# Performance work log

Measured on AMD Instinct MI355X. Metric: run time of the kernel, lower is better.

Reference implementation:

```python
import jax, jax.numpy as jnp
import numpy as np

N_NODES = 50000
N_EDGES = 65536
D_NODE = 1024
D_HID = 1024


def setup_inputs() -> dict:
    key = jax.random.key(0)
    k1, k2, k3, k4, k5 = jax.random.split(key, 5)
    node_feats = jax.random.normal(k1, (N_NODES, D_NODE), dtype=jnp.float32)
    src = jax.random.randint(k2, (N_EDGES,), 0, N_NODES, dtype=jnp.int64)
    dst = jax.random.randint(k3, (N_EDGES,), 0, N_NODES, dtype=jnp.int64)
    # MLP([2048, 1024, 1024]) with ReLU between layers, bias, no BN, no dropout
    W1 = jax.random.normal(k4, (2 * D_NODE, D_HID), dtype=jnp.float32) * (1.0 / np.sqrt(2 * D_NODE))
    b1 = jnp.zeros((D_HID,), dtype=jnp.float32)
    W2 = jax.random.normal(k5, (D_HID, D_HID), dtype=jnp.float32) * (1.0 / np.sqrt(D_HID))
    b2 = jnp.zeros((D_HID,), dtype=jnp.float32)
    return {"node_feats": node_feats, "src": src, "dst": dst,
            "W1": W1, "b1": b1, "W2": W2, "b2": b2}


def reference(node_feats, src, dst, W1, b1, W2, b2):
    # gather per-edge src/dst node features and concat: [E, 2d]
    feat = jnp.concatenate([node_feats[src], node_feats[dst]], axis=1)
    # edge MLP: Linear -> ReLU -> Linear
    h = jax.nn.relu(feat @ W1 + b1)
    e_f = h @ W2 + b2  # [E, D_HID]
    return e_f
```

## Files before the change

kernel.cpp:

```cpp
#include <hip/hip_runtime.h>
#include <stdint.h>
#include <stddef.h>

typedef unsigned short u16;
typedef __bf16 bf16_t;
typedef bf16_t bf16x8 __attribute__((ext_vector_type(8)));
typedef float f32x4 __attribute__((ext_vector_type(4)));
typedef u16 u16x4 __attribute__((ext_vector_type(4)));

#define N_NODES 50000
#define N_EDGES 65536
#define D_NODE 1024
#define D_HID 1024

#define BM 256
#define BK 64
#define BUFE (BM * BK)
#define LDS_BYTES (4 * BUFE * 2)


__device__ __forceinline__ u16 f2bf(float f) {
  union { float f; uint32_t u; } v; v.f = f;
  uint32_t u = v.u;
  u += 0x7FFF + ((u >> 16) & 1);
  return (u16)(u >> 16);
}

typedef __attribute__((address_space(1))) const void GV;
typedef __attribute__((address_space(3))) void LV;

__device__ __forceinline__ void gll16(const void* g, void* lds_wave_base) {
  __builtin_amdgcn_global_load_lds((GV*)g, (LV*)lds_wave_base, 16, 0, 0);
}


__global__ void detect_i64_kernel(const int* __restrict__ src, int* __restrict__ flag) {
  if (threadIdx.x == 0 && blockIdx.x == 0) {
    int o = 0;
    for (int i = 1; i < 32; i += 2) o |= src[i];
    *flag = (o == 0) ? 1 : 0;
  }
}

__global__ void cvt_bf16_kernel(const float* __restrict__ in, u16* __restrict__ out, size_t n4) {
  size_t i = (size_t)blockIdx.x * blockDim.x + threadIdx.x;
  if (i >= n4) return;
  float4 v = reinterpret_cast<const float4*>(in)[i];
  u16x4 o;
  o.x = f2bf(v.x); o.y = f2bf(v.y); o.z = f2bf(v.z); o.w = f2bf(v.w);
  reinterpret_cast<u16x4*>(out)[i] = o;
}

__global__ void transpose_cvt_kernel(const float* __restrict__ in, u16* __restrict__ out,
                                     int K, int N) {
  __shared__ float tile[32][33];
  int n0 = blockIdx.x * 32, k0 = blockIdx.y * 32;
  int tx = threadIdx.x, ty = threadIdx.y;
  #pragma unroll
  for (int i = ty; i < 32; i += 8)
    tile[i][tx] = in[(size_t)(k0 + i) * N + (n0 + tx)];
  __syncthreads();
  #pragma unroll
  for (int i = ty; i < 32; i += 8)
    out[(size_t)(n0 + i) * K + (k0 + tx)] = f2bf(tile[tx][i]);
}


#define PHASE_MFMA(i0, i1)                                                              \
  do {                                                                                  \
    _Pragma("unroll")                                                                   \
    for (int j = 0; j < 4; ++j) {                                                       \
      acc[i0][j] = __builtin_amdgcn_mfma_f32_16x16x32_bf16(afA[0], bfr[j][0], acc[i0][j], 0, 0, 0); \
      acc[i0][j] = __builtin_amdgcn_mfma_f32_16x16x32_bf16(afA[1], bfr[j][1], acc[i0][j], 0, 0, 0); \
    }                                                                                   \
    _Pragma("unroll")                                                                   \
    for (int j = 0; j < 4; ++j) {                                                       \
      acc[i1][j] = __builtin_amdgcn_mfma_f32_16x16x32_bf16(afB[0], bfr[j][0], acc[i1][j], 0, 0, 0); \
      acc[i1][j] = __builtin_amdgcn_mfma_f32_16x16x32_bf16(afB[1], bfr[j][1], acc[i1][j], 0, 0, 0); \
    }                                                                                   \
  } while (0)

#define LDA(dst, i, ks) \
  dst = *reinterpret_cast<const bf16x8*>(As_c + arow + (i) * 16 * BK + ((ks) ? kb1 : kb0))
#define LDB(j, ks) \
  bfr[j][ks] = *reinterpret_cast<const bf16x8*>(Bs_c + brow + (j) * 16 * BK + ((ks) ? kb1 : kb0))

template <bool FIRST>
__launch_bounds__(512, 2)
__global__ void gemm_kernel(const u16* __restrict__ Abf,
                            const int* __restrict__ src,
                            const int* __restrict__ dst,
                            const int* __restrict__ is64p,
                            const u16* __restrict__ Bt,
                            const float* __restrict__ bias,
                            u16* __restrict__ hout,
                            float* __restrict__ fout,
                            const int K) {
  extern __shared__ __align__(16) u16 lds[];
  u16* const ldsA = lds;
  u16* const ldsB = lds + 2 * BUFE;

  const int t = threadIdx.x;
  const int lane = t & 63;
  const int wave = t >> 6;

  const int b = blockIdx.x;
  const int wgid = (b & 7) * 128 + (b >> 3);
  const int bm = (wgid >> 2) * BM;
  const int bn = (wgid & 3) * BM;

  const int wm = (wave >> 2) * 128;
  const int wn = (wave & 3) * 64;

  const int srow = t >> 3;
  const int kswz = (((t & 7) ^ (srow & 7)) << 3);
  const int stoff = wave * 512;

  const u16* ap[4];
  const u16* ad[4];
  const u16* bp[4];
  if constexpr (FIRST) {
    const int is64 = *is64p;
    #pragma unroll
    for (int q = 0; q < 4; ++q) {
      const int e = bm + q * 64 + srow;
      const int s = is64 ? src[2 * e] : src[e];
      const int d = is64 ? dst[2 * e] : dst[e];
      ap[q] = Abf + (size_t)s * D_NODE + kswz;
      ad[q] = Abf + (size_t)d * D_NODE + kswz;
    }
  } else {
    #pragma unroll
    for (int q = 0; q < 4; ++q) {
      ap[q] = Abf + (size_t)(bm + q * 64 + srow) * K + kswz;
      ad[q] = nullptr;
    }
  }
  #pragma unroll
  for (int q = 0; q < 4; ++q)
    bp[q] = Bt + (size_t)(bn + q * 64 + srow) * K + kswz;

  auto stageA = [&](int buf, int q, int u) {
    const u16* g;
    if constexpr (FIRST) {
      g = (u < (D_NODE / BK)) ? (ap[q] + u * BK) : (ad[q] + (u - D_NODE / BK) * BK);
    } else {
      g = ap[q] + u * BK;
    }
    gll16(g, ldsA + buf * BUFE + q * 4096 + stoff);
  };
  auto stageB = [&](int buf, int q, int u) {
    gll16(bp[q] + u * BK, ldsB + buf * BUFE + q * 4096 + stoff);
  };

  const int lm = lane & 15;
  const int kq8 = ((lane >> 4) & 3) << 3;
  const int swzr = (lm & 7) << 3;
  const int kb0 = kq8 ^ swzr;
  const int kb1 = (32 + kq8) ^ swzr;
  const int arow = (wm + lm) * BK;
  const int brow = (wn + lm) * BK;

  f32x4 acc[8][4] = {};

  const int NT = K / BK;

  #pragma unroll
  for (int q = 0; q < 4; ++q) stageB(0, q, 0);
  #pragma unroll
  for (int q = 0; q < 4; ++q) stageA(0, q, 0);
  #pragma unroll
  for (int q = 0; q < 4; ++q) stageB(1, q, 1);
  stageA(1, 0, 1);
  stageA(1, 2, 1);
  asm volatile("s_waitcnt vmcnt(6)" ::: "memory");
  __builtin_amdgcn_s_barrier();

  for (int u = 0; u < NT; ++u) {
    const int cb = u & 1;
    const u16* As_c = ldsA + cb * BUFE;
    const u16* Bs_c = ldsB + cb * BUFE;

    bf16x8 bfr[4][2];
    bf16x8 afA[2], afB[2];

    #pragma unroll
    for (int j = 0; j < 4; ++j) { LDB(j, 0); LDB(j, 1); }
    LDA(afA[0], 0, 0); LDA(afA[1], 0, 1);
    LDA(afB[0], 1, 0); LDA(afB[1], 1, 1);
    if (u + 1 < NT) { stageA(cb ^ 1, 1, u + 1); stageA(cb ^ 1, 3, u + 1); }
    __builtin_amdgcn_s_barrier();
    asm volatile("s_waitcnt lgkmcnt(0)");
    __builtin_amdgcn_s_setprio(1);
    PHASE_MFMA(0, 1);
    __builtin_amdgcn_s_setprio(0);
    __builtin_amdgcn_s_barrier();

    LDA(afA[0], 2, 0); LDA(afA[1], 2, 1);
    LDA(afB[0], 3, 0); LDA(afB[1], 3, 1);
    if (u + 2 < NT) { stageB(cb, 0, u + 2); stageB(cb, 1, u + 2); }
    __builtin_amdgcn_s_barrier();
    asm volatile("s_waitcnt lgkmcnt(0)");
    __builtin_amdgcn_s_setprio(1);
    PHASE_MFMA(2, 3);
    __builtin_amdgcn_s_setprio(0);
    __builtin_amdgcn_s_barrier();

    LDA(afA[0], 4, 0); LDA(afA[1], 4, 1);
    LDA(afB[0], 5, 0); LDA(afB[1], 5, 1);
    if (u + 2 < NT) { stageB(cb, 2, u + 2); stageB(cb, 3, u + 2); }
    __builtin_amdgcn_s_barrier();
    asm volatile("s_waitcnt lgkmcnt(0)");
    __builtin_amdgcn_s_setprio(1);
    PHASE_MFMA(4, 5);
    __builtin_amdgcn_s_setprio(0);
    __builtin_amdgcn_s_barrier();

    LDA(afA[0], 6, 0); LDA(afA[1], 6, 1);
    LDA(afB[0], 7, 0); LDA(afB[1], 7, 1);
    if (u + 2 < NT) { stageA(cb, 0, u + 2); stageA(cb, 2, u + 2); }
    __builtin_amdgcn_s_barrier();
    asm volatile("s_waitcnt lgkmcnt(0)");
    __builtin_amdgcn_s_setprio(1);
    PHASE_MFMA(6, 7);
    __builtin_amdgcn_s_setprio(0);
    if (u + 2 < NT)      asm volatile("s_waitcnt vmcnt(6)" ::: "memory");
    else if (u + 1 < NT) asm volatile("s_waitcnt vmcnt(0)" ::: "memory");
    __builtin_amdgcn_s_barrier();
  }

  const int rq = ((lane >> 4) & 3) * 4;
  #pragma unroll
  for (int j = 0; j < 4; ++j) {
    const int n = bn + wn + 16 * j + lm;
    const float bj = bias[n];
    #pragma unroll
    for (int i = 0; i < 8; ++i) {
      const int m0 = bm + wm + 16 * i + rq;
      f32x4 c = acc[i][j];
      #pragma unroll
      for (int rr = 0; rr < 4; ++rr) {
        float v = c[rr] + bj;
        if (FIRST) {
          v = fmaxf(v, 0.0f);
          hout[(size_t)(m0 + rr) * D_HID + n] = f2bf(v);
        } else {
          fout[(size_t)(m0 + rr) * D_HID + n] = v;
        }
      }
    }
  }
}


extern "C" void kernel_launch(void* const* d_in, const int* in_sizes, int n_in,
                              void* d_out, int out_size, void* d_ws, size_t ws_size,
                              hipStream_t stream) {
  const float* node_feats = (const float*)d_in[0];
  const int*   src        = (const int*)d_in[1];
  const int*   dst        = (const int*)d_in[2];
  const float* W1         = (const float*)d_in[3];
  const float* b1         = (const float*)d_in[4];
  const float* W2         = (const float*)d_in[5];
  const float* b2         = (const float*)d_in[6];
  float* out = (float*)d_out;

  u16* ws = (u16*)d_ws;
  const size_t NODE_E = (size_t)N_NODES * D_NODE;
  u16* node_bf = ws;
  u16* W1T = node_bf + NODE_E;
  u16* W2T = W1T + (size_t)2048 * 1024;
  u16* h   = W2T + (size_t)1024 * 1024;
  int* flag = (int*)(h + (size_t)N_EDGES * D_HID);

  static bool attr_set = false;
  if (!attr_set) {
    hipFuncSetAttribute(reinterpret_cast<const void*>(&gemm_kernel<true>),
                        hipFuncAttributeMaxDynamicSharedMemorySize, LDS_BYTES);
    hipFuncSetAttribute(reinterpret_cast<const void*>(&gemm_kernel<false>),
                        hipFuncAttributeMaxDynamicSharedMemorySize, LDS_BYTES);
    attr_set = true;
  }

  detect_i64_kernel<<<1, 64, 0, stream>>>(src, flag);

  cvt_bf16_kernel<<<(unsigned)(NODE_E / 4 / 256), 256, 0, stream>>>(node_feats, node_bf, NODE_E / 4);

  transpose_cvt_kernel<<<dim3(1024 / 32, 2048 / 32), dim3(32, 8), 0, stream>>>(W1, W1T, 2048, 1024);
  transpose_cvt_kernel<<<dim3(1024 / 32, 1024 / 32), dim3(32, 8), 0, stream>>>(W2, W2T, 1024, 1024);

  gemm_kernel<true><<<1024, 512, LDS_BYTES, stream>>>(
      node_bf, src, dst, flag, W1T, b1, h, nullptr, 2 * D_NODE);

  gemm_kernel<false><<<1024, 512, LDS_BYTES, stream>>>(
      h, nullptr, nullptr, nullptr, W2T, b2, nullptr, out, D_HID);
}
```

Baseline: 822.0 us.

## Simplify GEMM main loop to single-barrier double buffering with one-tile prefetch

Replaces the four-phase interleaved schedule with a simpler loop. The old loop had several barriers per K-tile and a two-tile-ahead prefetch. The new loop issues all A and B global-to-LDS loads for the next tile at the top of the iteration, then runs the MFMAs in three groups split by K-half, and ends with a full vmcnt(0) wait and one barrier. The goal is to cut barrier and synchronisation overhead. The cost is shallower prefetch depth, and global loads are no longer interleaved with compute phases, so gather latency may be exposed. The templated kernel is also wrapped into two non-template entry kernels.

```diff
diff --git a/kernel.cpp b/kernel.cpp
--- a/kernel.cpp
+++ b/kernel.cpp
@@ -66,36 +66,16 @@
 }
 
 
-#define PHASE_MFMA(i0, i1)                                                              \
-  do {                                                                                  \
-    _Pragma("unroll")                                                                   \
-    for (int j = 0; j < 4; ++j) {                                                       \
-      acc[i0][j] = __builtin_amdgcn_mfma_f32_16x16x32_bf16(afA[0], bfr[j][0], acc[i0][j], 0, 0, 0); \
-      acc[i0][j] = __builtin_amdgcn_mfma_f32_16x16x32_bf16(afA[1], bfr[j][1], acc[i0][j], 0, 0, 0); \
-    }                                                                                   \
-    _Pragma("unroll")                                                                   \
-    for (int j = 0; j < 4; ++j) {                                                       \
-      acc[i1][j] = __builtin_amdgcn_mfma_f32_16x16x32_bf16(afB[0], bfr[j][0], acc[i1][j], 0, 0, 0); \
-      acc[i1][j] = __builtin_amdgcn_mfma_f32_16x16x32_bf16(afB[1], bfr[j][1], acc[i1][j], 0, 0, 0); \
-    }                                                                                   \
-  } while (0)
-
-#define LDA(dst, i, ks) \
-  dst = *reinterpret_cast<const bf16x8*>(As_c + arow + (i) * 16 * BK + ((ks) ? kb1 : kb0))
-#define LDB(j, ks) \
-  bfr[j][ks] = *reinterpret_cast<const bf16x8*>(Bs_c + brow + (j) * 16 * BK + ((ks) ? kb1 : kb0))
-
 template <bool FIRST>
-__launch_bounds__(512, 2)
-__global__ void gemm_kernel(const u16* __restrict__ Abf,
-                            const int* __restrict__ src,
-                            const int* __restrict__ dst,
-                            const int* __restrict__ is64p,
-                            const u16* __restrict__ Bt,
-                            const float* __restrict__ bias,
-                            u16* __restrict__ hout,
-                            float* __restrict__ fout,
-                            const int K) {
+__device__ __forceinline__ void gemm_body(const u16* __restrict__ Abf,
+                                          const int* __restrict__ src,
+                                          const int* __restrict__ dst,
+                                          const int* __restrict__ is64p,
+                                          const u16* __restrict__ Bt,
+                                          const float* __restrict__ bias,
+                                          u16* __restrict__ hout,
+                                          float* __restrict__ fout,
+                                          const int K) {
   extern __shared__ __align__(16) u16 lds[];
   u16* const ldsA = lds;
   u16* const ldsB = lds + 2 * BUFE;
@@ -166,14 +146,10 @@
   const int NT = K / BK;
 
   #pragma unroll
+  for (int q = 0; q < 4; ++q) stageA(0, q, 0);
+  #pragma unroll
   for (int q = 0; q < 4; ++q) stageB(0, q, 0);
-  #pragma unroll
-  for (int q = 0; q < 4; ++q) stageA(0, q, 0);
-  #pragma unroll
-  for (int q = 0; q < 4; ++q) stageB(1, q, 1);
-  stageA(1, 0, 1);
-  stageA(1, 2, 1);
-  asm volatile("s_waitcnt vmcnt(6)" ::: "memory");
+  asm volatile("s_waitcnt vmcnt(0)" ::: "memory");
   __builtin_amdgcn_s_barrier();
 
   for (int u = 0; u < NT; ++u) {
@@ -181,51 +157,67 @@
     const u16* As_c = ldsA + cb * BUFE;
     const u16* Bs_c = ldsB + cb * BUFE;
 
-    bf16x8 bfr[4][2];
-    bf16x8 afA[2], afB[2];
-
-    #pragma unroll
-    for (int j = 0; j < 4; ++j) { LDB(j, 0); LDB(j, 1); }
-    LDA(afA[0], 0, 0); LDA(afA[1], 0, 1);
-    LDA(afB[0], 1, 0); LDA(afB[1], 1, 1);
-    if (u + 1 < NT) { stageA(cb ^ 1, 1, u + 1); stageA(cb ^ 1, 3, u + 1); }
-    __builtin_amdgcn_s_barrier();
-    asm volatile("s_waitcnt lgkmcnt(0)");
+    if (u + 1 < NT) {
+      const int nb = cb ^ 1;
+      stageA(nb, 0, u + 1); stageA(nb, 1, u + 1);
+      stageA(nb, 2, u + 1); stageA(nb, 3, u + 1);
+      stageB(nb, 0, u + 1); stageB(nb, 1, u + 1);
+      stageB(nb, 2, u + 1); stageB(nb, 3, u + 1);
+    }
+
+    bf16x8 aq[4], ar[4], bq[4], br[4];
+
+    #pragma unroll
+    for (int j = 0; j < 4; ++j)
+      bq[j] = *reinterpret_cast<const bf16x8*>(Bs_c + brow + j * 1024 + kb0);
+    #pragma unroll
+    for (int i = 0; i < 4; ++i)
+      aq[i] = *reinterpret_cast<const bf16x8*>(As_c + arow + i * 1024 + kb0);
+    #pragma unroll
+    for (int i = 0; i < 4; ++i)
+      ar[i] = *reinterpret_cast<const bf16x8*>(As_c + arow + (i + 4) * 1024 + kb0);
+
     __builtin_amdgcn_s_setprio(1);
-    PHASE_MFMA(0, 1);
+    #pragma unroll
+    for (int i = 0; i < 4; ++i)
+      #pragma unroll
+      for (int j = 0; j < 4; ++j)
+        acc[i][j] = __builtin_amdgcn_mfma_f32_16x16x32_bf16(aq[i], bq[j], acc[i][j], 0, 0, 0);
     __builtin_amdgcn_s_setprio(0);
-    __builtin_amdgcn_s_barrier();
-
-    LDA(afA[0], 2, 0); LDA(afA[1], 2, 1);
-    LDA(afB[0], 3, 0); LDA(afB[1], 3, 1);
-    if (u + 2 < NT) { stageB(cb, 0, u + 2); stageB(cb, 1, u + 2); }
-    __builtin_amdgcn_s_barrier();
-    asm volatile("s_waitcnt lgkmcnt(0)");
+
+    #pragma unroll
+    for (int j = 0; j < 4; ++j)
+      br[j] = *reinterpret_cast<const bf16x8*>(Bs_c + brow + j * 1024 + kb1);
+    #pragma unroll
+    for (int i = 0; i < 4; ++i)
+      aq[i] = *reinterpret_cast<const bf16x8*>(As_c + arow + i * 1024 + kb1);
+
     __builtin_amdgcn_s_setprio(1);
-    PHASE_MFMA(2, 3);
+    #pragma unroll
+    for (int i = 0; i < 4; ++i)
+      #pragma unroll
+      for (int j = 0; j < 4; ++j)
+        acc[i + 4][j] = __builtin_amdgcn_mfma_f32_16x16x32_bf16(ar[i], bq[j], acc[i + 4][j], 0, 0, 0);
     __builtin_amdgcn_s_setprio(0);
-    __builtin_amdgcn_s_barrier();
-
-    LDA(afA[0], 4, 0); LDA(afA[1], 4, 1);
-    LDA(afB[0], 5, 0); LDA(afB[1], 5, 1);
-    if (u + 2 < NT) { stageB(cb, 2, u + 2); stageB(cb, 3, u + 2); }
-    __builtin_amdgcn_s_barrier();
-    asm volatile("s_waitcnt lgkmcnt(0)");
+
+    #pragma unroll
+    for (int i = 0; i < 4; ++i)
+      ar[i] = *reinterpret_cast<const bf16x8*>(As_c + arow + (i + 4) * 1024 + kb1);
+
     __builtin_amdgcn_s_setprio(1);
-    PHASE_MFMA(4, 5);
+    #pragma unroll
+    for (int i = 0; i < 4; ++i)
+      #pragma unroll
+      for (int j = 0; j < 4; ++j)
+        acc[i][j] = __builtin_amdgcn_mfma_f32_16x16x32_bf16(aq[i], br[j], acc[i][j], 0, 0, 0);
+    #pragma unroll
+    for (int i = 0; i < 4; ++i)
+      #pragma unroll
+      for (int j = 0; j < 4; ++j)
+        acc[i + 4][j] = __builtin_amdgcn_mfma_f32_16x16x32_bf16(ar[i], br[j], acc[i + 4][j], 0, 0, 0);
     __builtin_amdgcn_s_setprio(0);
-    __builtin_amdgcn_s_barrier();
-
-    LDA(afA[0], 6, 0); LDA(afA[1], 6, 1);
-    LDA(afB[0], 7, 0); LDA(afB[1], 7, 1);
-    if (u + 2 < NT) { stageA(cb, 0, u + 2); stageA(cb, 2, u + 2); }
-    __builtin_amdgcn_s_barrier();
-    asm volatile("s_waitcnt lgkmcnt(0)");
-    __builtin_amdgcn_s_setprio(1);
-    PHASE_MFMA(6, 7);
-    __builtin_amdgcn_s_setprio(0);
-    if (u + 2 < NT)      asm volatile("s_waitcnt vmcnt(6)" ::: "memory");
-    else if (u + 1 < NT) asm volatile("s_waitcnt vmcnt(0)" ::: "memory");
+
+    asm volatile("s_waitcnt vmcnt(0)" ::: "memory");
     __builtin_amdgcn_s_barrier();
   }
 
@@ -240,16 +232,30 @@
       f32x4 c = acc[i][j];
       #pragma unroll
       for (int rr = 0; rr < 4; ++rr) {
-        float v = c[rr] + bj;
+        float vv = c[rr] + bj;
         if (FIRST) {
-          v = fmaxf(v, 0.0f);
-          hout[(size_t)(m0 + rr) * D_HID + n] = f2bf(v);
+          vv = fmaxf(vv, 0.0f);
+          hout[(size_t)(m0 + rr) * D_HID + n] = f2bf(vv);
         } else {
-          fout[(size_t)(m0 + rr) * D_HID + n] = v;
+          fout[(size_t)(m0 + rr) * D_HID + n] = vv;
         }
       }
     }
   }
+}
+
+__launch_bounds__(512, 2)
+__global__ void gemm1_kernel(const u16* __restrict__ Abf, const int* __restrict__ src,
+                             const int* __restrict__ dst, const int* __restrict__ is64p,
+                             const u16* __restrict__ Bt, const float* __restrict__ bias,
+                             u16* __restrict__ hout) {
+  gemm_body<true>(Abf, src, dst, is64p, Bt, bias, hout, nullptr, 2 * D_NODE);
+}
+
+__launch_bounds__(512, 2)
+__global__ void gemm2_kernel(const u16* __restrict__ Abf, const u16* __restrict__ Bt,
+                             const float* __restrict__ bias, float* __restrict__ fout) {
+  gemm_body<false>(Abf, nullptr, nullptr, nullptr, Bt, bias, nullptr, fout, D_HID);
 }
 
 
@@ -275,9 +281,9 @@
 
   static bool attr_set = false;
   if (!attr_set) {
-    hipFuncSetAttribute(reinterpret_cast<const void*>(&gemm_kernel<true>),
+    hipFuncSetAttribute(reinterpret_cast<const void*>(&gemm1_kernel),
                         hipFuncAttributeMaxDynamicSharedMemorySize, LDS_BYTES);
-    hipFuncSetAttribute(reinterpret_cast<const void*>(&gemm_kernel<false>),
+    hipFuncSetAttribute(reinterpret_cast<const void*>(&gemm2_kernel),
                         hipFuncAttributeMaxDynamicSharedMemorySize, LDS_BYTES);
     attr_set = true;
   }
@@ -289,9 +295,7 @@
   transpose_cvt_kernel<<<dim3(1024 / 32, 2048 / 32), dim3(32, 8), 0, stream>>>(W1, W1T, 2048, 1024);
   transpose_cvt_kernel<<<dim3(1024 / 32, 1024 / 32), dim3(32, 8), 0, stream>>>(W2, W2T, 1024, 1024);
 
-  gemm_kernel<true><<<1024, 512, LDS_BYTES, stream>>>(
-      node_bf, src, dst, flag, W1T, b1, h, nullptr, 2 * D_NODE);
-
-  gemm_kernel<false><<<1024, 512, LDS_BYTES, stream>>>(
-      h, nullptr, nullptr, nullptr, W2T, b2, nullptr, out, D_HID);
-}
+  gemm1_kernel<<<1024, 512, LDS_BYTES, stream>>>(node_bf, src, dst, flag, W1T, b1, h);
+
+  gemm2_kernel<<<1024, 512, LDS_BYTES, stream>>>(h, W2T, b2, out);
+}
```

Result: faster. 804.8 us (-2.1%).
